# Kernel tuning notes

Measured on AMD Instinct MI355X. Metric: run time of the kernel, lower is better.

## Reference

```python
import jax, jax.numpy as jnp
import numpy as np
from jax import lax

SENT_LEN = 32      # fixed sentence length used to build sent_id -> max packed length
MD = 128           # max_distance


def setup_inputs() -> dict:
    key = jax.random.key(0)
    ks = jax.random.split(key, 14)
    W, H, D, HID, E, CC, K = 4096, 2048, 768, 1024, 64, 64, 3
    PAIR = 2 * D + E  # 1600
    words = jax.random.normal(ks[0], (W, D), dtype=jnp.float32)
    sent_id = (jnp.arange(W, dtype=jnp.int32) // SENT_LEN)
    heads_ids = jax.random.randint(ks[1], (H,), 0, W, dtype=jnp.int32)
    emb_table = jax.random.normal(ks[2], (MD, E), dtype=jnp.float32) * 0.02
    w1 = jax.random.normal(ks[3], (PAIR, HID), dtype=jnp.float32) * 0.02
    b1 = jnp.zeros((HID,), jnp.float32)
    w2 = jax.random.normal(ks[4], (HID, 256), dtype=jnp.float32) * 0.02
    b2 = jnp.zeros((256,), jnp.float32)
    w3 = jax.random.normal(ks[5], (256, E), dtype=jnp.float32) * 0.02
    b3 = jnp.zeros((E,), jnp.float32)
    conv1_w = jax.random.normal(ks[6], (CC, E, K), dtype=jnp.float32) * 0.05
    conv1_b = jnp.zeros((CC,), jnp.float32)
    conv2_w = jax.random.normal(ks[7], (2, CC, K), dtype=jnp.float32) * 0.05
    conv2_b = jnp.zeros((2,), jnp.float32)
    return {"sent_id": sent_id, "words": words, "heads_ids": heads_ids,
            "emb_table": emb_table, "w1": w1, "b1": b1, "w2": w2, "b2": b2,
            "w3": w3, "b3": b3, "conv1_w": conv1_w, "conv1_b": conv1_b,
            "conv2_w": conv2_w, "conv2_b": conv2_b}


def _conv1d(x, w, b):
    # x: [N, C, L], w: [O, I, K], hardcoded padding=1 like the torch module
    y = lax.conv_general_dilated(x, w, (1,), [(1, 1)],
                                 dimension_numbers=("NCH", "OIH", "NCH"))
    return y + b[None, :, None]


def reference(sent_id, words, heads_ids, emb_table, w1, b1, w2, b2, w3, b3,
              conv1_w, conv1_b, conv2_w, conv2_b):
    H = heads_ids.shape[0]
    W = words.shape[0]
    rows = jnp.arange(H)[:, None]
    # same-sentence mask [H, W] and packed slot per column
    mask_full = sent_id[heads_ids][:, None] == sent_id[None, :]
    pos = jnp.cumsum(mask_full.astype(jnp.int32), axis=1) - 1
    slot = jnp.where(mask_full, pos, SENT_LEN)          # OOB -> dropped
    # col_idx[h, p] = word index at packed slot p (sentinel W if empty)
    col_idx = jnp.full((H, SENT_LEN), W, dtype=jnp.int32)
    col_idx = col_idx.at[rows, slot].set(
        jnp.broadcast_to(jnp.arange(W, dtype=jnp.int32)[None, :], (H, W)),
        mode="drop")
    mask = col_idx < W                                   # [H, SENT_LEN]
    cols = jnp.minimum(col_idx, W - 1)
    # gather pair features: [head feats | word feats | dist emb]
    head_w = words[heads_ids]                            # [H, D]
    word_w = words[cols]                                 # [H, L, D]
    rel = heads_ids[:, None].astype(jnp.int32) - cols    # relative positions
    eid = rel + (MD - 2) // 2
    eid = jnp.where((eid < 0) | (eid > MD - 2), MD - 1, eid)
    pairs = jnp.concatenate([
        jnp.broadcast_to(head_w[:, None, :], (H, SENT_LEN, head_w.shape[-1])),
        word_w, emb_table[eid]], axis=-1)
    pairs = jnp.where(mask[..., None], pairs, 0.0)       # torch zero padding
    # FFNN (eval mode: dropout is identity)
    x = jax.nn.relu(pairs @ w1 + b1)
    x = jax.nn.relu(x @ w2 + b2)
    x = x @ w3 + b3                                       # [H, L, E]
    # conv stack over packed word axis
    y = _conv1d(x.transpose(0, 2, 1), conv1_w, conv1_b)
    y = _conv1d(y, conv2_w, conv2_b)
    res = y.transpose(0, 2, 1)                            # [H, L, 2]
    # scatter back into full score tensor
    scores = jnp.full((H, W, 2), -jnp.inf, dtype=res.dtype)
    scores = scores.at[rows, col_idx].set(res, mode="drop")
    # eval-mode validity masks
    rel_full = heads_ids[:, None].astype(jnp.int32) - jnp.arange(W, dtype=jnp.int32)[None, :]
    valid_starts = jnp.log((rel_full >= 0).astype(scores.dtype))
    valid_ends = jnp.log((rel_full <= 0).astype(scores.dtype))
    return scores + jnp.stack([valid_starts, valid_ends], axis=2)
```

## Files before the change

kernel.cpp:

```cpp
#include <hip/hip_runtime.h>
#include <cstddef>
#include <cstdint>

#define NEG_SENT (-1.0e30f)


typedef short s8v __attribute__((ext_vector_type(8)));
typedef float f32x4 __attribute__((ext_vector_type(4)));

static __device__ __forceinline__ f32x4 mfma16(s8v a, s8v b, f32x4 c) {
  return __builtin_amdgcn_mfma_f32_16x16x32_bf16(a, b, c, 0, 0, 0);
}
static __device__ __forceinline__ unsigned short f2b(float f) {
  union { float f; unsigned u; } v{f};
  unsigned r = v.u + 0x7FFF + ((v.u >> 16) & 1);
  return (unsigned short)(r >> 16);
}
static __device__ __forceinline__ float b2f(unsigned short u) {
  union { unsigned u; float f; } v{((unsigned)u) << 16};
  return v.f;
}

__global__ __launch_bounds__(256) void k_embC(const float* __restrict__ emb,
                                              const float* __restrict__ w1,
                                              const float* __restrict__ b1,
                                              float* __restrict__ embC) {
  const int e = blockIdx.x, t = threadIdx.x;
  __shared__ float se[64];
  if (t < 64) se[t] = emb[e * 64 + t];
  __syncthreads();
  float4 acc = *reinterpret_cast<const float4*>(b1 + 4 * t);
#pragma unroll 8
  for (int d = 0; d < 64; ++d) {
    const float4 wv =
        *reinterpret_cast<const float4*>(w1 + (size_t)(1536 + d) * 1024 + 4 * t);
    const float a = se[d];
    acc.x += a * wv.x; acc.y += a * wv.y; acc.z += a * wv.z; acc.w += a * wv.w;
  }
  *reinterpret_cast<float4*>(embC + (size_t)e * 1024 + 4 * t) = acc;
}

__global__ __launch_bounds__(256) void k_cvt_words(const float* __restrict__ A,
                                                   s8v* __restrict__ AF) {
  const int tid = blockIdx.x * 256 + threadIdx.x;
  const int lane = tid & 63, ks = (tid >> 6) % 24, mt = tid / 1536;
  const int m = mt * 16 + (lane & 15);
  const int kb = ks * 32 + 8 * (lane >> 4);
  const float* src = A + (size_t)m * 768 + kb;
  const float4 v0 = *reinterpret_cast<const float4*>(src);
  const float4 v1 = *reinterpret_cast<const float4*>(src + 4);
  s8v p;
  p[0] = (short)f2b(v0.x); p[1] = (short)f2b(v0.y);
  p[2] = (short)f2b(v0.z); p[3] = (short)f2b(v0.w);
  p[4] = (short)f2b(v1.x); p[5] = (short)f2b(v1.y);
  p[6] = (short)f2b(v1.z); p[7] = (short)f2b(v1.w);
  AF[tid] = p;
}

__global__ __launch_bounds__(256) void k_cvt_w1(const float* __restrict__ w1,
                                                s8v* __restrict__ BF) {
  const int tid = blockIdx.x * 256 + threadIdx.x;
  const int lane = tid & 63, ks = (tid >> 6) % 24, nt = tid / 1536;
  const int n = nt * 16 + (lane & 15);
  const int kb = ks * 32 + 8 * (lane >> 4);
  const int z = n >> 10, col = n & 1023;
  const float* src = w1 + (size_t)(z * 768 + kb) * 1024 + col;
  s8v p;
#pragma unroll
  for (int j = 0; j < 8; ++j) p[j] = (short)f2b(src[(size_t)j * 1024]);
  BF[tid] = p;
}

__global__ __launch_bounds__(256) void k_cvt_small(const float* __restrict__ w2,
                                                   const float* __restrict__ w3,
                                                   const float* __restrict__ c1w,
                                                   s8v* __restrict__ w2F,
                                                   s8v* __restrict__ w3F,
                                                   s8v* __restrict__ c1F) {
  const int b = blockIdx.x, t = threadIdx.x;
  if (b < 128) {
    const int tid = b * 256 + t;
    const int lane = tid & 63, ks = (tid >> 6) % 32, nt = tid / 2048;
    const int n = nt * 16 + (lane & 15);
    const int kb = ks * 32 + 8 * (lane >> 4);
    s8v p;
#pragma unroll
    for (int j = 0; j < 8; ++j) p[j] = (short)f2b(w2[(size_t)(kb + j) * 256 + n]);
    w2F[tid] = p;
  } else if (b < 136) {
    const int tid = (b - 128) * 256 + t;
    const int lane = tid & 63, ks = (tid >> 6) % 8, nt = tid / 512;
    const int n = nt * 16 + (lane & 15);
    const int kb = ks * 32 + 8 * (lane >> 4);
    s8v p;
#pragma unroll
    for (int j = 0; j < 8; ++j) p[j] = (short)f2b(w3[(size_t)(kb + j) * 64 + n]);
    w3F[tid] = p;
  } else {
    const int tid = (b - 136) * 256 + t;
    const int lane = tid & 63, ks = (tid >> 6) % 6, nt = tid / 384;
    const int o = nt * 16 + (lane & 15);
    const int kb = ks * 32 + 8 * (lane >> 4);
    s8v p;
#pragma unroll
    for (int j = 0; j < 8; ++j) {
      const int k = kb + j, tap = k >> 6, c = k & 63;
      p[j] = (short)f2b(c1w[(size_t)(o * 64 + c) * 3 + tap]);
    }
    c1F[tid] = p;
  }
}

__global__ __launch_bounds__(256) void k_gemm1b(const s8v* __restrict__ AF,
                                                const s8v* __restrict__ BF,
                                                unsigned short* __restrict__ AWb) {
  const int t = threadIdx.x, lane = t & 63, w = t >> 6;
  const int mq = w & 1, nq = w >> 1;
  const int mt0 = blockIdx.y * 8 + mq * 4;
  const int nt0 = blockIdx.x * 8 + nq * 4;
  f32x4 acc[4][4] = {};
  const s8v* Ab = AF + (size_t)mt0 * 24 * 64 + lane;
  const s8v* Bb = BF + (size_t)nt0 * 24 * 64 + lane;
#pragma unroll 2
  for (int ks = 0; ks < 24; ++ks) {
    s8v a[4], bx[4];
#pragma unroll
    for (int i = 0; i < 4; ++i) a[i] = Ab[(size_t)(i * 24 + ks) * 64];
#pragma unroll
    for (int j = 0; j < 4; ++j) bx[j] = Bb[(size_t)(j * 24 + ks) * 64];
#pragma unroll
    for (int i = 0; i < 4; ++i)
#pragma unroll
      for (int j = 0; j < 4; ++j) acc[i][j] = mfma16(a[i], bx[j], acc[i][j]);
  }
  const int rl = (lane >> 4) * 4, cl = lane & 15;
#pragma unroll
  for (int i = 0; i < 4; ++i)
#pragma unroll
    for (int j = 0; j < 4; ++j) {
      const int n = (nt0 + j) * 16 + cl;
#pragma unroll
      for (int r = 0; r < 4; ++r) {
        const int m = (mt0 + i) * 16 + rl + r;
        AWb[(size_t)m * 2048 + n] = f2b(acc[i][j][r]);
      }
    }
}

__global__ __launch_bounds__(256) void k_fused(
    const int* __restrict__ heads, const unsigned short* __restrict__ AWb,
    const float* __restrict__ embC, const s8v* __restrict__ w2F,
    const float* __restrict__ b2, const s8v* __restrict__ w3F,
    const float* __restrict__ b3, const s8v* __restrict__ c1F,
    const float* __restrict__ c1b, const float* __restrict__ c2w,
    const float* __restrict__ c2b, float* __restrict__ out) {
  const int h = blockIdx.x, t = threadIdx.x;
  const int lane = t & 63, w = t >> 6;
  const int hid = heads[h];
  const int s = hid >> 5, off = hid & 31;

  __shared__ float sHead[1024];
  __shared__ s8v sA[2][4][64];
  __shared__ s8v sX2f[2][8][64];
  __shared__ float sX3[34][68];
  __shared__ float sY1[34][68];
  __shared__ s8v sAc[2][6][64];

  {
    float4 m4; m4.x = m4.y = m4.z = m4.w = NEG_SENT;
    float4* orow = reinterpret_cast<float4*>(out + (size_t)h * 8192);
#pragma unroll
    for (int i = 0; i < 8; ++i) {
      const int fi = t + (i << 8);
      if ((fi >> 4) != s) orow[fi] = m4;
    }
  }
  if (t < 68) { sX3[0][t] = 0.f; sX3[33][t] = 0.f; sY1[0][t] = 0.f; sY1[33][t] = 0.f; }

  {
    const ushort4 hv = *reinterpret_cast<const ushort4*>(AWb + (size_t)hid * 2048 + 4 * t);
    float4 hf; hf.x = b2f(hv.x); hf.y = b2f(hv.y); hf.z = b2f(hv.z); hf.w = b2f(hv.w);
    *reinterpret_cast<float4*>(&sHead[4 * t]) = hf;
  }

  const int rp = t >> 3;
  const int kb = (t & 7) * 16;
  const int eidp = off - rp + 63;
  const unsigned short* wrow = AWb + (size_t)(s * 32 + rp) * 2048 + 1024 + kb;
  const float* erow = embC + (size_t)eidp * 1024 + kb;
  const int smt = rp >> 4;
  const int sl0 = (rp & 15) + 16 * ((kb >> 3) & 3);
  const int sl1 = (rp & 15) + 16 * (((kb + 8) >> 3) & 3);

  f32x4 acc2[2][4] = {};
  const s8v* w2b = w2F + (size_t)(w * 4) * 32 * 64 + lane;

  for (int j0 = 0; j0 < 1024; j0 += 128) {
    __syncthreads();
    {
      const uint4 wv0 = *reinterpret_cast<const uint4*>(wrow + j0);
      const uint4 wv1 = *reinterpret_cast<const uint4*>(wrow + j0 + 8);
      const float4 e0 = *reinterpret_cast<const float4*>(erow + j0);
      const float4 e1 = *reinterpret_cast<const float4*>(erow + j0 + 4);
      const float4 e2 = *reinterpret_cast<const float4*>(erow + j0 + 8);
      const float4 e3 = *reinterpret_cast<const float4*>(erow + j0 + 12);
      const float4 h0 = *reinterpret_cast<const float4*>(&sHead[j0 + kb]);
      const float4 h1 = *reinterpret_cast<const float4*>(&sHead[j0 + kb + 4]);
      const float4 h2 = *reinterpret_cast<const float4*>(&sHead[j0 + kb + 8]);
      const float4 h3 = *reinterpret_cast<const float4*>(&sHead[j0 + kb + 12]);
      const unsigned wu[4] = {wv0.x, wv0.y, wv0.z, wv0.w};
      const unsigned wu2[4] = {wv1.x, wv1.y, wv1.z, wv1.w};
      const float ee[16] = {e0.x, e0.y, e0.z, e0.w, e1.x, e1.y, e1.z, e1.w,
                            e2.x, e2.y, e2.z, e2.w, e3.x, e3.y, e3.z, e3.w};
      const float hh[16] = {h0.x, h0.y, h0.z, h0.w, h1.x, h1.y, h1.z, h1.w,
                            h2.x, h2.y, h2.z, h2.w, h3.x, h3.y, h3.z, h3.w};
      s8v p0, p1;
#pragma unroll
      for (int j = 0; j < 8; ++j) {
        const unsigned u = (j & 1) ? (wu[j >> 1] >> 16) : (wu[j >> 1] & 0xffff);
        p0[j] = (short)f2b(fmaxf(b2f((unsigned short)u) + ee[j] + hh[j], 0.f));
      }
#pragma unroll
      for (int j = 0; j < 8; ++j) {
        const unsigned u = (j & 1) ? (wu2[j >> 1] >> 16) : (wu2[j >> 1] & 0xffff);
        p1[j] = (short)f2b(fmaxf(b2f((unsigned short)u) + ee[8 + j] + hh[8 + j], 0.f));
      }
      sA[smt][kb >> 5][sl0] = p0;
      sA[smt][(kb + 8) >> 5][sl1] = p1;
    }
    __syncthreads();

    const int kg0 = j0 >> 5;
#pragma unroll
    for (int ks = 0; ks < 4; ++ks) {
      const s8v a0 = sA[0][ks][lane];
      const s8v a1 = sA[1][ks][lane];
#pragma unroll
      for (int nt = 0; nt < 4; ++nt) {
        const s8v bfr = w2b[(size_t)(nt * 32 + kg0 + ks) * 64];
        acc2[0][nt] = mfma16(a0, bfr, acc2[0][nt]);
        acc2[1][nt] = mfma16(a1, bfr, acc2[1][nt]);
      }
    }
  }

  {
    unsigned short* sX2u = reinterpret_cast<unsigned short*>(&sX2f[0][0][0]);
    const int rl = (lane >> 4) * 4, cl = lane & 15;
#pragma unroll
    for (int nt = 0; nt < 4; ++nt) {
      const int n = 64 * w + 16 * nt + cl;
      const float bv = b2[n];
      const int ksx = n >> 5;
      const int lgrp = 16 * ((n >> 3) & 3);
      const int idx = n & 7;
#pragma unroll
      for (int mt = 0; mt < 2; ++mt)
#pragma unroll
        for (int r = 0; r < 4; ++r) {
          const int m = 16 * mt + rl + r;
          const float v = fmaxf(acc2[mt][nt][r] + bv, 0.f);
          sX2u[(((size_t)mt * 8 + ksx) * 64 + (m & 15) + lgrp) * 8 + idx] = f2b(v);
        }
    }
  }
  __syncthreads();

  {
    f32x4 acc3[2] = {};
    const s8v* w3b = w3F + (size_t)(w * 8) * 64 + lane;
#pragma unroll
    for (int ks = 0; ks < 8; ++ks) {
      const s8v bfr = w3b[(size_t)ks * 64];
      acc3[0] = mfma16(sX2f[0][ks][lane], bfr, acc3[0]);
      acc3[1] = mfma16(sX2f[1][ks][lane], bfr, acc3[1]);
    }
    const int rl = (lane >> 4) * 4, n = 16 * w + (lane & 15);
    const float bv = b3[n];
#pragma unroll
    for (int mt = 0; mt < 2; ++mt)
#pragma unroll
      for (int r = 0; r < 4; ++r) sX3[1 + 16 * mt + rl + r][n] = acc3[mt][r] + bv;
  }
  __syncthreads();

#pragma unroll
  for (int u = 0; u < 3; ++u) {
    const int sl = t + 256 * u;
    const int mt = sl / 384, rem = sl - mt * 384;
    const int ks = rem >> 6, ln = rem & 63;
    const int kbb = 32 * ks + 8 * (ln >> 4);
    const int tap = kbb >> 6, c = kbb & 63;
    const int m = 16 * mt + (ln & 15);
    const float4 v0 = *reinterpret_cast<const float4*>(&sX3[m + tap][c]);
    const float4 v1 = *reinterpret_cast<const float4*>(&sX3[m + tap][c + 4]);
    s8v p;
    p[0] = (short)f2b(v0.x); p[1] = (short)f2b(v0.y);
    p[2] = (short)f2b(v0.z); p[3] = (short)f2b(v0.w);
    p[4] = (short)f2b(v1.x); p[5] = (short)f2b(v1.y);
    p[6] = (short)f2b(v1.z); p[7] = (short)f2b(v1.w);
    sAc[mt][ks][ln] = p;
  }
  __syncthreads();

  {
    f32x4 accc[2] = {};
    const s8v* c1bp = c1F + (size_t)(w * 6) * 64 + lane;
#pragma unroll
    for (int ks = 0; ks < 6; ++ks) {
      const s8v bfr = c1bp[(size_t)ks * 64];
      accc[0] = mfma16(sAc[0][ks][lane], bfr, accc[0]);
      accc[1] = mfma16(sAc[1][ks][lane], bfr, accc[1]);
    }
    const int rl = (lane >> 4) * 4, o = 16 * w + (lane & 15);
    const float bv = c1b[o];
#pragma unroll
    for (int mt = 0; mt < 2; ++mt)
#pragma unroll
      for (int r = 0; r < 4; ++r) sY1[1 + 16 * mt + rl + r][o] = accc[mt][r] + bv;
  }
  __syncthreads();

  {
    const int c2 = t >> 7, p = (t >> 2) & 31, kq = t & 3;
    float acc = 0.f;
#pragma unroll
    for (int ci = 16 * kq; ci < 16 * kq + 16; ++ci) {
      const float w0 = c2w[(size_t)(c2 * 64 + ci) * 3 + 0];
      const float w1v = c2w[(size_t)(c2 * 64 + ci) * 3 + 1];
      const float w2v = c2w[(size_t)(c2 * 64 + ci) * 3 + 2];
      acc += sY1[p][ci] * w0 + sY1[p + 1][ci] * w1v + sY1[p + 2][ci] * w2v;
    }
    acc += __shfl_xor(acc, 1, 64);
    acc += __shfl_xor(acc, 2, 64);
    if (kq == 0) {
      const int rel = off - p;
      const bool ok = (c2 == 0) ? (rel >= 0) : (rel <= 0);
      out[(size_t)h * 8192 + (size_t)(s * 32 + p) * 2 + c2] =
          ok ? (acc + c2b[c2]) : NEG_SENT;
    }
  }
}

extern "C" void kernel_launch(void* const* d_in, const int* in_sizes, int n_in,
                              void* d_out, int out_size, void* d_ws,
                              size_t ws_size, hipStream_t stream) {
  const float* words = (const float*)d_in[1];
  const int* heads = (const int*)d_in[2];
  const float* emb = (const float*)d_in[3];
  const float* w1 = (const float*)d_in[4];
  const float* b1 = (const float*)d_in[5];
  const float* w2 = (const float*)d_in[6];
  const float* b2 = (const float*)d_in[7];
  const float* w3 = (const float*)d_in[8];
  const float* b3 = (const float*)d_in[9];
  const float* c1w = (const float*)d_in[10];
  const float* c1b = (const float*)d_in[11];
  const float* c2w = (const float*)d_in[12];
  const float* c2b = (const float*)d_in[13];
  float* out = (float*)d_out;

  char* ws = (char*)d_ws;
  float* embC = (float*)ws;                         ws += 128 * 1024 * 4;
  unsigned short* AWb = (unsigned short*)ws;        ws += 4096 * 2048 * 2;
  s8v* wordsF = (s8v*)ws;                           ws += 393216 * 16;
  s8v* w1F = (s8v*)ws;                              ws += 196608 * 16;
  s8v* w2F = (s8v*)ws;                              ws += 32768 * 16;
  s8v* w3F = (s8v*)ws;                              ws += 2048 * 16;
  s8v* c1F = (s8v*)ws;                              ws += 1536 * 16;

  k_embC<<<128, 256, 0, stream>>>(emb, w1, b1, embC);
  k_cvt_words<<<1536, 256, 0, stream>>>(words, wordsF);
  k_cvt_w1<<<768, 256, 0, stream>>>(w1, w1F);
  k_cvt_small<<<142, 256, 0, stream>>>(w2, w3, c1w, w2F, w3F, c1F);
  k_gemm1b<<<dim3(16, 32), 256, 0, stream>>>(wordsF, w1F, AWb);
  k_fused<<<2048, 256, 0, stream>>>(heads, AWb, embC, w2F, b2, w3F, b3, c1F,
                                    c1b, c2w, c2b, out);
}
```

Measured before the change: 252.1 us.

## Process two heads per block in fused kernel and merge prep kernels

The fused per-head kernel now handles two heads per block (64 packed rows), swapping MFMA operand roles so each weight fragment of w2, w3 and conv1 is reused across both heads. Shared memory is folded into one aliased region, packed bf16 conversion is used on gfx950, and occupancy is hinted with launch bounds. The four preprocessing kernels are merged into one launch to cut launch overhead. The cost is more registers and accumulators per thread and a more intricate shared-memory layout.

```diff
diff --git a/kernel.cpp b/kernel.cpp
--- a/kernel.cpp
+++ b/kernel.cpp
@@ -20,94 +20,102 @@
   union { unsigned u; float f; } v{((unsigned)u) << 16};
   return v.f;
 }
-
-__global__ __launch_bounds__(256) void k_embC(const float* __restrict__ emb,
-                                              const float* __restrict__ w1,
-                                              const float* __restrict__ b1,
-                                              float* __restrict__ embC) {
-  const int e = blockIdx.x, t = threadIdx.x;
+static __device__ __forceinline__ unsigned pk2(float a, float b) {
+#if defined(__gfx950__) && __has_builtin(__builtin_amdgcn_cvt_pk_bf16_f32)
+  typedef __bf16 b2t __attribute__((ext_vector_type(2)));
+  b2t r = __builtin_amdgcn_cvt_pk_bf16_f32(a, b);
+  return __builtin_bit_cast(unsigned, r);
+#else
+  return (unsigned)f2b(a) | ((unsigned)f2b(b) << 16);
+#endif
+}
+static __device__ __forceinline__ float blo(unsigned u) {
+  union { unsigned u; float f; } v{u << 16}; return v.f;
+}
+static __device__ __forceinline__ float bhi(unsigned u) {
+  union { unsigned u; float f; } v{u & 0xffff0000u}; return v.f;
+}
+
+__global__ __launch_bounds__(256) void k_prep(
+    const float* __restrict__ words, const float* __restrict__ w1,
+    const float* __restrict__ b1, const float* __restrict__ emb,
+    const float* __restrict__ w2, const float* __restrict__ w3,
+    const float* __restrict__ c1w, s8v* __restrict__ wordsF,
+    s8v* __restrict__ w1F, s8v* __restrict__ w2F, s8v* __restrict__ w3F,
+    s8v* __restrict__ c1F, float* __restrict__ embC) {
+  const int bb = blockIdx.x, t = threadIdx.x;
   __shared__ float se[64];
-  if (t < 64) se[t] = emb[e * 64 + t];
-  __syncthreads();
-  float4 acc = *reinterpret_cast<const float4*>(b1 + 4 * t);
-#pragma unroll 8
-  for (int d = 0; d < 64; ++d) {
-    const float4 wv =
-        *reinterpret_cast<const float4*>(w1 + (size_t)(1536 + d) * 1024 + 4 * t);
-    const float a = se[d];
-    acc.x += a * wv.x; acc.y += a * wv.y; acc.z += a * wv.z; acc.w += a * wv.w;
-  }
-  *reinterpret_cast<float4*>(embC + (size_t)e * 1024 + 4 * t) = acc;
-}
-
-__global__ __launch_bounds__(256) void k_cvt_words(const float* __restrict__ A,
-                                                   s8v* __restrict__ AF) {
-  const int tid = blockIdx.x * 256 + threadIdx.x;
-  const int lane = tid & 63, ks = (tid >> 6) % 24, mt = tid / 1536;
-  const int m = mt * 16 + (lane & 15);
-  const int kb = ks * 32 + 8 * (lane >> 4);
-  const float* src = A + (size_t)m * 768 + kb;
-  const float4 v0 = *reinterpret_cast<const float4*>(src);
-  const float4 v1 = *reinterpret_cast<const float4*>(src + 4);
-  s8v p;
-  p[0] = (short)f2b(v0.x); p[1] = (short)f2b(v0.y);
-  p[2] = (short)f2b(v0.z); p[3] = (short)f2b(v0.w);
-  p[4] = (short)f2b(v1.x); p[5] = (short)f2b(v1.y);
-  p[6] = (short)f2b(v1.z); p[7] = (short)f2b(v1.w);
-  AF[tid] = p;
-}
-
-__global__ __launch_bounds__(256) void k_cvt_w1(const float* __restrict__ w1,
-                                                s8v* __restrict__ BF) {
-  const int tid = blockIdx.x * 256 + threadIdx.x;
-  const int lane = tid & 63, ks = (tid >> 6) % 24, nt = tid / 1536;
-  const int n = nt * 16 + (lane & 15);
-  const int kb = ks * 32 + 8 * (lane >> 4);
-  const int z = n >> 10, col = n & 1023;
-  const float* src = w1 + (size_t)(z * 768 + kb) * 1024 + col;
-  s8v p;
-#pragma unroll
-  for (int j = 0; j < 8; ++j) p[j] = (short)f2b(src[(size_t)j * 1024]);
-  BF[tid] = p;
-}
-
-__global__ __launch_bounds__(256) void k_cvt_small(const float* __restrict__ w2,
-                                                   const float* __restrict__ w3,
-                                                   const float* __restrict__ c1w,
-                                                   s8v* __restrict__ w2F,
-                                                   s8v* __restrict__ w3F,
-                                                   s8v* __restrict__ c1F) {
-  const int b = blockIdx.x, t = threadIdx.x;
-  if (b < 128) {
-    const int tid = b * 256 + t;
-    const int lane = tid & 63, ks = (tid >> 6) % 32, nt = tid / 2048;
+  if (bb < 1536) {
+    const int tid = bb * 256 + t;
+    const int lane = tid & 63, ks = (tid >> 6) % 24, mt = tid / 1536;
+    const int m = mt * 16 + (lane & 15);
+    const int kb = ks * 32 + 8 * (lane >> 4);
+    const float* src = words + (size_t)m * 768 + kb;
+    const float4 v0 = *reinterpret_cast<const float4*>(src);
+    const float4 v1 = *reinterpret_cast<const float4*>(src + 4);
+    s8v p;
+    p[0] = (short)f2b(v0.x); p[1] = (short)f2b(v0.y);
+    p[2] = (short)f2b(v0.z); p[3] = (short)f2b(v0.w);
+    p[4] = (short)f2b(v1.x); p[5] = (short)f2b(v1.y);
+    p[6] = (short)f2b(v1.z); p[7] = (short)f2b(v1.w);
+    wordsF[tid] = p;
+  } else if (bb < 2304) {
+    const int tid = (bb - 1536) * 256 + t;
+    const int lane = tid & 63, ks = (tid >> 6) % 24, nt = tid / 1536;
     const int n = nt * 16 + (lane & 15);
     const int kb = ks * 32 + 8 * (lane >> 4);
+    const int z = n >> 10, col = n & 1023;
+    const float* src = w1 + (size_t)(z * 768 + kb) * 1024 + col;
     s8v p;
 #pragma unroll
-    for (int j = 0; j < 8; ++j) p[j] = (short)f2b(w2[(size_t)(kb + j) * 256 + n]);
-    w2F[tid] = p;
-  } else if (b < 136) {
-    const int tid = (b - 128) * 256 + t;
-    const int lane = tid & 63, ks = (tid >> 6) % 8, nt = tid / 512;
-    const int n = nt * 16 + (lane & 15);
-    const int kb = ks * 32 + 8 * (lane >> 4);
-    s8v p;
-#pragma unroll
-    for (int j = 0; j < 8; ++j) p[j] = (short)f2b(w3[(size_t)(kb + j) * 64 + n]);
-    w3F[tid] = p;
+    for (int j = 0; j < 8; ++j) p[j] = (short)f2b(src[(size_t)j * 1024]);
+    w1F[tid] = p;
+  } else if (bb < 2446) {
+    const int b = bb - 2304;
+    if (b < 128) {
+      const int tid = b * 256 + t;
+      const int lane = tid & 63, ks = (tid >> 6) % 32, nt = tid / 2048;
+      const int n = nt * 16 + (lane & 15);
+      const int kb = ks * 32 + 8 * (lane >> 4);
+      s8v p;
+#pragma unroll
+      for (int j = 0; j < 8; ++j) p[j] = (short)f2b(w2[(size_t)(kb + j) * 256 + n]);
+      w2F[tid] = p;
+    } else if (b < 136) {
+      const int tid = (b - 128) * 256 + t;
+      const int lane = tid & 63, ks = (tid >> 6) % 8, nt = tid / 512;
+      const int n = nt * 16 + (lane & 15);
+      const int kb = ks * 32 + 8 * (lane >> 4);
+      s8v p;
+#pragma unroll
+      for (int j = 0; j < 8; ++j) p[j] = (short)f2b(w3[(size_t)(kb + j) * 64 + n]);
+      w3F[tid] = p;
+    } else {
+      const int tid = (b - 136) * 256 + t;
+      const int lane = tid & 63, ks = (tid >> 6) % 6, nt = tid / 384;
+      const int o = nt * 16 + (lane & 15);
+      const int kb = ks * 32 + 8 * (lane >> 4);
+      s8v p;
+#pragma unroll
+      for (int j = 0; j < 8; ++j) {
+        const int k = kb + j, tap = k >> 6, c = k & 63;
+        p[j] = (short)f2b(c1w[(size_t)(o * 64 + c) * 3 + tap]);
+      }
+      c1F[tid] = p;
+    }
   } else {
-    const int tid = (b - 136) * 256 + t;
-    const int lane = tid & 63, ks = (tid >> 6) % 6, nt = tid / 384;
-    const int o = nt * 16 + (lane & 15);
-    const int kb = ks * 32 + 8 * (lane >> 4);
-    s8v p;
-#pragma unroll
-    for (int j = 0; j < 8; ++j) {
-      const int k = kb + j, tap = k >> 6, c = k & 63;
-      p[j] = (short)f2b(c1w[(size_t)(o * 64 + c) * 3 + tap]);
-    }
-    c1F[tid] = p;
+    const int e = bb - 2446;
+    if (t < 64) se[t] = emb[e * 64 + t];
+    __syncthreads();
+    float4 acc = *reinterpret_cast<const float4*>(b1 + 4 * t);
+#pragma unroll 8
+    for (int d = 0; d < 64; ++d) {
+      const float4 wv =
+          *reinterpret_cast<const float4*>(w1 + (size_t)(1536 + d) * 1024 + 4 * t);
+      const float a = se[d];
+      acc.x += a * wv.x; acc.y += a * wv.y; acc.z += a * wv.z; acc.w += a * wv.w;
+    }
+    *reinterpret_cast<float4*>(embC + (size_t)e * 1024 + 4 * t) = acc;
   }
 }
 
@@ -147,197 +155,213 @@
     }
 }
 
-__global__ __launch_bounds__(256) void k_fused(
+__global__ __launch_bounds__(256, 3) void k_fused(
     const int* __restrict__ heads, const unsigned short* __restrict__ AWb,
     const float* __restrict__ embC, const s8v* __restrict__ w2F,
     const float* __restrict__ b2, const s8v* __restrict__ w3F,
     const float* __restrict__ b3, const s8v* __restrict__ c1F,
     const float* __restrict__ c1b, const float* __restrict__ c2w,
     const float* __restrict__ c2b, float* __restrict__ out) {
-  const int h = blockIdx.x, t = threadIdx.x;
-  const int lane = t & 63, w = t >> 6;
-  const int hid = heads[h];
-  const int s = hid >> 5, off = hid & 31;
-
-  __shared__ float sHead[1024];
-  __shared__ s8v sA[2][4][64];
-  __shared__ s8v sX2f[2][8][64];
-  __shared__ float sX3[34][68];
-  __shared__ float sY1[34][68];
-  __shared__ s8v sAc[2][6][64];
+  const int h0 = blockIdx.x * 2;
+  const int t = threadIdx.x, lane = t & 63, w = t >> 6;
+  const int q = lane >> 4, cl = lane & 15;
+  const int hidA = heads[h0], hidB = heads[h0 + 1];
+  const int sA_ = hidA >> 5, offA = hidA & 31;
+  const int sB_ = hidB >> 5, offB = hidB & 31;
+
+  __shared__ float sHead[2][1024];
+  __shared__ __align__(16) char regA[32768];
+  s8v (*sB1)[4][64] = reinterpret_cast<s8v(*)[4][64]>(regA);
+  s8v (*sX2f)[8][64] = reinterpret_cast<s8v(*)[8][64]>(regA);
+  s8v (*sCv)[6][64] = reinterpret_cast<s8v(*)[6][64]>(regA);
+  float* sY1 = reinterpret_cast<float*>(regA);
+  ushort* sX2u = reinterpret_cast<ushort*>(regA);
 
   {
     float4 m4; m4.x = m4.y = m4.z = m4.w = NEG_SENT;
-    float4* orow = reinterpret_cast<float4*>(out + (size_t)h * 8192);
+    float4* o0 = reinterpret_cast<float4*>(out + (size_t)h0 * 8192);
+    float4* o1 = reinterpret_cast<float4*>(out + (size_t)(h0 + 1) * 8192);
 #pragma unroll
     for (int i = 0; i < 8; ++i) {
       const int fi = t + (i << 8);
-      if ((fi >> 4) != s) orow[fi] = m4;
-    }
-  }
-  if (t < 68) { sX3[0][t] = 0.f; sX3[33][t] = 0.f; sY1[0][t] = 0.f; sY1[33][t] = 0.f; }
-
-  {
-    const ushort4 hv = *reinterpret_cast<const ushort4*>(AWb + (size_t)hid * 2048 + 4 * t);
-    float4 hf; hf.x = b2f(hv.x); hf.y = b2f(hv.y); hf.z = b2f(hv.z); hf.w = b2f(hv.w);
-    *reinterpret_cast<float4*>(&sHead[4 * t]) = hf;
-  }
-
-  const int rp = t >> 3;
-  const int kb = (t & 7) * 16;
-  const int eidp = off - rp + 63;
-  const unsigned short* wrow = AWb + (size_t)(s * 32 + rp) * 2048 + 1024 + kb;
-  const float* erow = embC + (size_t)eidp * 1024 + kb;
-  const int smt = rp >> 4;
-  const int sl0 = (rp & 15) + 16 * ((kb >> 3) & 3);
-  const int sl1 = (rp & 15) + 16 * (((kb + 8) >> 3) & 3);
-
-  f32x4 acc2[2][4] = {};
-  const s8v* w2b = w2F + (size_t)(w * 4) * 32 * 64 + lane;
+      if ((fi >> 4) != sA_) o0[fi] = m4;
+      if ((fi >> 4) != sB_) o1[fi] = m4;
+    }
+  }
+
+  {
+    const ushort4 ha = *reinterpret_cast<const ushort4*>(AWb + (size_t)hidA * 2048 + 4 * t);
+    const ushort4 hb = *reinterpret_cast<const ushort4*>(AWb + (size_t)hidB * 2048 + 4 * t);
+    float4 fa; fa.x = b2f(ha.x); fa.y = b2f(ha.y); fa.z = b2f(ha.z); fa.w = b2f(ha.w);
+    float4 fb; fb.x = b2f(hb.x); fb.y = b2f(hb.y); fb.z = b2f(hb.z); fb.w = b2f(hb.w);
+    *reinterpret_cast<float4*>(&sHead[0][4 * t]) = fa;
+    *reinterpret_cast<float4*>(&sHead[1][4 * t]) = fb;
+  }
+
+  const int pprime = t >> 2;
+  const int kb32 = (t & 3) * 32;
+  const int headS = pprime >> 5, posS = pprime & 31;
+  const int hidS = headS ? hidB : hidA;
+  const int offS = hidS & 31;
+  const int eidp = offS - posS + 63;
+  const unsigned short* wrow =
+      AWb + (size_t)((hidS >> 5) * 32 + posS) * 2048 + 1024 + kb32;
+  const float* erow = embC + (size_t)eidp * 1024 + kb32;
+  const float* hrow = &sHead[headS][kb32];
+  const int ntp0 = pprime >> 4, ksS = t & 3, l0 = pprime & 15;
+
+  f32x4 acc[4][4] = {};
 
   for (int j0 = 0; j0 < 1024; j0 += 128) {
     __syncthreads();
-    {
-      const uint4 wv0 = *reinterpret_cast<const uint4*>(wrow + j0);
-      const uint4 wv1 = *reinterpret_cast<const uint4*>(wrow + j0 + 8);
-      const float4 e0 = *reinterpret_cast<const float4*>(erow + j0);
-      const float4 e1 = *reinterpret_cast<const float4*>(erow + j0 + 4);
-      const float4 e2 = *reinterpret_cast<const float4*>(erow + j0 + 8);
-      const float4 e3 = *reinterpret_cast<const float4*>(erow + j0 + 12);
-      const float4 h0 = *reinterpret_cast<const float4*>(&sHead[j0 + kb]);
-      const float4 h1 = *reinterpret_cast<const float4*>(&sHead[j0 + kb + 4]);
-      const float4 h2 = *reinterpret_cast<const float4*>(&sHead[j0 + kb + 8]);
-      const float4 h3 = *reinterpret_cast<const float4*>(&sHead[j0 + kb + 12]);
-      const unsigned wu[4] = {wv0.x, wv0.y, wv0.z, wv0.w};
-      const unsigned wu2[4] = {wv1.x, wv1.y, wv1.z, wv1.w};
-      const float ee[16] = {e0.x, e0.y, e0.z, e0.w, e1.x, e1.y, e1.z, e1.w,
-                            e2.x, e2.y, e2.z, e2.w, e3.x, e3.y, e3.z, e3.w};
-      const float hh[16] = {h0.x, h0.y, h0.z, h0.w, h1.x, h1.y, h1.z, h1.w,
-                            h2.x, h2.y, h2.z, h2.w, h3.x, h3.y, h3.z, h3.w};
-      s8v p0, p1;
-#pragma unroll
-      for (int j = 0; j < 8; ++j) {
-        const unsigned u = (j & 1) ? (wu[j >> 1] >> 16) : (wu[j >> 1] & 0xffff);
-        p0[j] = (short)f2b(fmaxf(b2f((unsigned short)u) + ee[j] + hh[j], 0.f));
+#pragma unroll
+    for (int g = 0; g < 4; ++g) {
+      const uint4 wv = *reinterpret_cast<const uint4*>(wrow + j0 + 8 * g);
+      const float4 e0 = *reinterpret_cast<const float4*>(erow + j0 + 8 * g);
+      const float4 e1 = *reinterpret_cast<const float4*>(erow + j0 + 8 * g + 4);
+      const float4 g0 = *reinterpret_cast<const float4*>(hrow + j0 + 8 * g);
+      const float4 g1 = *reinterpret_cast<const float4*>(hrow + j0 + 8 * g + 4);
+      uint4 r;
+      r.x = pk2(fmaxf(blo(wv.x) + e0.x + g0.x, 0.f),
+                fmaxf(bhi(wv.x) + e0.y + g0.y, 0.f));
+      r.y = pk2(fmaxf(blo(wv.y) + e0.z + g0.z, 0.f),
+                fmaxf(bhi(wv.y) + e0.w + g0.w, 0.f));
+      r.z = pk2(fmaxf(blo(wv.z) + e1.x + g1.x, 0.f),
+                fmaxf(bhi(wv.z) + e1.y + g1.y, 0.f));
+      r.w = pk2(fmaxf(blo(wv.w) + e1.z + g1.z, 0.f),
+                fmaxf(bhi(wv.w) + e1.w + g1.w, 0.f));
+      *reinterpret_cast<uint4*>(&sB1[ntp0][ksS][l0 + 16 * g]) = r;
+    }
+    __syncthreads();
+
+    const int ksg0 = j0 >> 5;
+#pragma unroll
+    for (int ks2 = 0; ks2 < 4; ++ks2) {
+      s8v bv[4], av[4];
+#pragma unroll
+      for (int ntp = 0; ntp < 4; ++ntp) bv[ntp] = sB1[ntp][ks2][lane];
+#pragma unroll
+      for (int i = 0; i < 4; ++i)
+        av[i] = w2F[(size_t)((w * 4 + i) * 32 + ksg0 + ks2) * 64 + lane];
+#pragma unroll
+      for (int i = 0; i < 4; ++i)
+#pragma unroll
+        for (int ntp = 0; ntp < 4; ++ntp)
+          acc[i][ntp] = mfma16(av[i], bv[ntp], acc[i][ntp]);
+    }
+  }
+  __syncthreads();
+
+#pragma unroll
+  for (int i = 0; i < 4; ++i) {
+    const int n2b = w * 64 + i * 16 + q * 4;
+    const float4 bb = *reinterpret_cast<const float4*>(b2 + n2b);
+    const int ks3 = n2b >> 5, g3 = (n2b >> 3) & 3, idx0 = n2b & 7;
+#pragma unroll
+    for (int ntp = 0; ntp < 4; ++ntp) {
+      const unsigned u0 = pk2(fmaxf(acc[i][ntp][0] + bb.x, 0.f),
+                              fmaxf(acc[i][ntp][1] + bb.y, 0.f));
+      const unsigned u1 = pk2(fmaxf(acc[i][ntp][2] + bb.z, 0.f),
+                              fmaxf(acc[i][ntp][3] + bb.w, 0.f));
+      uint2 uu; uu.x = u0; uu.y = u1;
+      *reinterpret_cast<uint2*>(
+          sX2u + (((size_t)ntp * 8 + ks3) * 64 + cl + 16 * g3) * 8 + idx0) = uu;
+    }
+  }
+  __syncthreads();
+
+  f32x4 acc3[4] = {};
+#pragma unroll
+  for (int ks3 = 0; ks3 < 8; ++ks3) {
+    const s8v a = w3F[(size_t)(w * 8 + ks3) * 64 + lane];
+#pragma unroll
+    for (int ntp = 0; ntp < 4; ++ntp)
+      acc3[ntp] = mfma16(a, sX2f[ntp][ks3][lane], acc3[ntp]);
+  }
+  __syncthreads();
+
+  {
+    uint4 z; z.x = z.y = z.z = z.w = 0;
+    uint4* zp = reinterpret_cast<uint4*>(regA);
+#pragma unroll
+    for (int i2 = 0; i2 < 6; ++i2) zp[t + 256 * i2] = z;
+  }
+  __syncthreads();
+
+  {
+    const int cb = 16 * w + q * 4;
+    const float4 b3v = *reinterpret_cast<const float4*>(b3 + cb);
+    const int gC = (cb >> 3) & 3, idx0 = cb & 7, ksb = cb >> 5;
+#pragma unroll
+    for (int ntp = 0; ntp < 4; ++ntp) {
+      const int pp = ntp * 16 + cl, hd = pp >> 5, pos = pp & 31;
+      const unsigned u0 = pk2(acc3[ntp][0] + b3v.x, acc3[ntp][1] + b3v.y);
+      const unsigned u1 = pk2(acc3[ntp][2] + b3v.z, acc3[ntp][3] + b3v.w);
+      uint2 uu; uu.x = u0; uu.y = u1;
+#pragma unroll
+      for (int tau = 0; tau < 3; ++tau) {
+        const int pt = pos + 1 - tau;
+        if ((unsigned)pt < 32u) {
+          const int ppt = hd * 32 + pt;
+          const int ks = 2 * tau + ksb;
+          *reinterpret_cast<uint2*>(
+              sX2u + (((size_t)(ppt >> 4) * 6 + ks) * 64 + (ppt & 15) + 16 * gC) * 8 +
+              idx0) = uu;
+        }
       }
-#pragma unroll
-      for (int j = 0; j < 8; ++j) {
-        const unsigned u = (j & 1) ? (wu2[j >> 1] >> 16) : (wu2[j >> 1] & 0xffff);
-        p1[j] = (short)f2b(fmaxf(b2f((unsigned short)u) + ee[8 + j] + hh[8 + j], 0.f));
-      }
-      sA[smt][kb >> 5][sl0] = p0;
-      sA[smt][(kb + 8) >> 5][sl1] = p1;
-    }
-    __syncthreads();
-
-    const int kg0 = j0 >> 5;
-#pragma unroll
-    for (int ks = 0; ks < 4; ++ks) {
-      const s8v a0 = sA[0][ks][lane];
-      const s8v a1 = sA[1][ks][lane];
-#pragma unroll
-      for (int nt = 0; nt < 4; ++nt) {
-        const s8v bfr = w2b[(size_t)(nt * 32 + kg0 + ks) * 64];
-        acc2[0][nt] = mfma16(a0, bfr, acc2[0][nt]);
-        acc2[1][nt] = mfma16(a1, bfr, acc2[1][nt]);
-      }
-    }
-  }
-
-  {
-    unsigned short* sX2u = reinterpret_cast<unsigned short*>(&sX2f[0][0][0]);
-    const int rl = (lane >> 4) * 4, cl = lane & 15;
-#pragma unroll
-    for (int nt = 0; nt < 4; ++nt) {
-      const int n = 64 * w + 16 * nt + cl;
-      const float bv = b2[n];
-      const int ksx = n >> 5;
-      const int lgrp = 16 * ((n >> 3) & 3);
-      const int idx = n & 7;
-#pragma unroll
-      for (int mt = 0; mt < 2; ++mt)
-#pragma unroll
-        for (int r = 0; r < 4; ++r) {
-          const int m = 16 * mt + rl + r;
-          const float v = fmaxf(acc2[mt][nt][r] + bv, 0.f);
-          sX2u[(((size_t)mt * 8 + ksx) * 64 + (m & 15) + lgrp) * 8 + idx] = f2b(v);
-        }
-    }
-  }
-  __syncthreads();
-
-  {
-    f32x4 acc3[2] = {};
-    const s8v* w3b = w3F + (size_t)(w * 8) * 64 + lane;
-#pragma unroll
-    for (int ks = 0; ks < 8; ++ks) {
-      const s8v bfr = w3b[(size_t)ks * 64];
-      acc3[0] = mfma16(sX2f[0][ks][lane], bfr, acc3[0]);
-      acc3[1] = mfma16(sX2f[1][ks][lane], bfr, acc3[1]);
-    }
-    const int rl = (lane >> 4) * 4, n = 16 * w + (lane & 15);
-    const float bv = b3[n];
-#pragma unroll
-    for (int mt = 0; mt < 2; ++mt)
-#pragma unroll
-      for (int r = 0; r < 4; ++r) sX3[1 + 16 * mt + rl + r][n] = acc3[mt][r] + bv;
-  }
-  __syncthreads();
-
-#pragma unroll
-  for (int u = 0; u < 3; ++u) {
-    const int sl = t + 256 * u;
-    const int mt = sl / 384, rem = sl - mt * 384;
-    const int ks = rem >> 6, ln = rem & 63;
-    const int kbb = 32 * ks + 8 * (ln >> 4);
-    const int tap = kbb >> 6, c = kbb & 63;
-    const int m = 16 * mt + (ln & 15);
-    const float4 v0 = *reinterpret_cast<const float4*>(&sX3[m + tap][c]);
-    const float4 v1 = *reinterpret_cast<const float4*>(&sX3[m + tap][c + 4]);
-    s8v p;
-    p[0] = (short)f2b(v0.x); p[1] = (short)f2b(v0.y);
-    p[2] = (short)f2b(v0.z); p[3] = (short)f2b(v0.w);
-    p[4] = (short)f2b(v1.x); p[5] = (short)f2b(v1.y);
-    p[6] = (short)f2b(v1.z); p[7] = (short)f2b(v1.w);
-    sAc[mt][ks][ln] = p;
-  }
-  __syncthreads();
-
-  {
-    f32x4 accc[2] = {};
-    const s8v* c1bp = c1F + (size_t)(w * 6) * 64 + lane;
-#pragma unroll
-    for (int ks = 0; ks < 6; ++ks) {
-      const s8v bfr = c1bp[(size_t)ks * 64];
-      accc[0] = mfma16(sAc[0][ks][lane], bfr, accc[0]);
-      accc[1] = mfma16(sAc[1][ks][lane], bfr, accc[1]);
-    }
-    const int rl = (lane >> 4) * 4, o = 16 * w + (lane & 15);
-    const float bv = c1b[o];
-#pragma unroll
-    for (int mt = 0; mt < 2; ++mt)
-#pragma unroll
-      for (int r = 0; r < 4; ++r) sY1[1 + 16 * mt + rl + r][o] = accc[mt][r] + bv;
-  }
-  __syncthreads();
-
-  {
-    const int c2 = t >> 7, p = (t >> 2) & 31, kq = t & 3;
-    float acc = 0.f;
-#pragma unroll
-    for (int ci = 16 * kq; ci < 16 * kq + 16; ++ci) {
-      const float w0 = c2w[(size_t)(c2 * 64 + ci) * 3 + 0];
-      const float w1v = c2w[(size_t)(c2 * 64 + ci) * 3 + 1];
-      const float w2v = c2w[(size_t)(c2 * 64 + ci) * 3 + 2];
-      acc += sY1[p][ci] * w0 + sY1[p + 1][ci] * w1v + sY1[p + 2][ci] * w2v;
-    }
-    acc += __shfl_xor(acc, 1, 64);
-    acc += __shfl_xor(acc, 2, 64);
+    }
+  }
+  __syncthreads();
+
+  f32x4 accc[4] = {};
+#pragma unroll
+  for (int ks = 0; ks < 6; ++ks) {
+    const s8v a = c1F[(size_t)(w * 6 + ks) * 64 + lane];
+#pragma unroll
+    for (int ntp = 0; ntp < 4; ++ntp)
+      accc[ntp] = mfma16(a, sCv[ntp][ks][lane], accc[ntp]);
+  }
+  __syncthreads();
+
+  {
+    const int o = t >> 2, pc = t & 3;
+    const int colz = (pc == 0) ? 0 : (pc == 1) ? 33 : (pc == 2) ? 34 : 67;
+    sY1[o * 68 + colz] = 0.f;
+  }
+  {
+    const int ob = 16 * w + q * 4;
+    const float4 cbv = *reinterpret_cast<const float4*>(c1b + ob);
+#pragma unroll
+    for (int ntp = 0; ntp < 4; ++ntp) {
+      const int pp = ntp * 16 + cl, hd = pp >> 5, pos = pp & 31;
+      const int col = hd * 34 + 1 + pos;
+      sY1[(ob + 0) * 68 + col] = accc[ntp][0] + cbv.x;
+      sY1[(ob + 1) * 68 + col] = accc[ntp][1] + cbv.y;
+      sY1[(ob + 2) * 68 + col] = accc[ntp][2] + cbv.z;
+      sY1[(ob + 3) * 68 + col] = accc[ntp][3] + cbv.w;
+    }
+  }
+  __syncthreads();
+
+  {
+    const int kq = t & 1, c2 = (t >> 1) & 1, pp = t >> 2;
+    const int hd = pp >> 5, pos = pp & 31, col = hd * 34 + 1 + pos;
+    float a2 = 0.f;
+    const float* wp = c2w + (size_t)(c2 * 64 + kq * 32) * 3;
+    const float* yb = sY1 + (size_t)(kq * 32) * 68 + col;
+#pragma unroll
+    for (int o = 0; o < 32; ++o) {
+      a2 += yb[o * 68 - 1] * wp[o * 3 + 0] + yb[o * 68] * wp[o * 3 + 1] +
+            yb[o * 68 + 1] * wp[o * 3 + 2];
+    }
+    a2 += __shfl_xor(a2, 1, 64);
     if (kq == 0) {
-      const int rel = off - p;
+      const int hidR = hd ? hidB : hidA;
+      const int sR = hidR >> 5, offR = hidR & 31;
+      const int rel = offR - pos;
       const bool ok = (c2 == 0) ? (rel >= 0) : (rel <= 0);
-      out[(size_t)h * 8192 + (size_t)(s * 32 + p) * 2 + c2] =
-          ok ? (acc + c2b[c2]) : NEG_SENT;
+      out[(size_t)(h0 + hd) * 8192 + (size_t)(sR * 32 + pos) * 2 + c2] =
+          ok ? (a2 + c2b[c2]) : NEG_SENT;
     }
   }
 }
@@ -369,11 +393,9 @@
   s8v* w3F = (s8v*)ws;                              ws += 2048 * 16;
   s8v* c1F = (s8v*)ws;                              ws += 1536 * 16;
 
-  k_embC<<<128, 256, 0, stream>>>(emb, w1, b1, embC);
-  k_cvt_words<<<1536, 256, 0, stream>>>(words, wordsF);
-  k_cvt_w1<<<768, 256, 0, stream>>>(w1, w1F);
-  k_cvt_small<<<142, 256, 0, stream>>>(w2, w3, c1w, w2F, w3F, c1F);
+  k_prep<<<2574, 256, 0, stream>>>(words, w1, b1, emb, w2, w3, c1w, wordsF,
+                                   w1F, w2F, w3F, c1F, embC);
   k_gemm1b<<<dim3(16, 32), 256, 0, stream>>>(wordsF, w1F, AWb);
-  k_fused<<<2048, 256, 0, stream>>>(heads, AWb, embC, w2F, b2, w3F, b3, c1F,
+  k_fused<<<1024, 256, 0, stream>>>(heads, AWb, embC, w2F, b2, w3F, b3, c1F,
                                     c1b, c2w, c2b, out);
 }
```

After: 264.7 us. 5.0% more time.
